# Optimization experiments

Measured on AMD Instinct MI355X. Metric: run time of the kernel, lower is better.

Reference implementation:

```python
import jax, jax.numpy as jnp
import numpy as np

D_MODEL = 1024
HEADS = 16
HEAD_DIM = D_MODEL // HEADS


def setup_inputs() -> dict:
    key = jax.random.key(0)
    k_x, k_q, k_k, k_v, k_o = jax.random.split(key, 5)
    B, S = 4, 2048
    return {
        "x": jax.random.normal(k_x, (B, S, D_MODEL), dtype=jnp.float32),
        "W_q": jax.random.normal(k_q, (D_MODEL, D_MODEL), dtype=jnp.float32),
        "W_k": jax.random.normal(k_k, (D_MODEL, D_MODEL), dtype=jnp.float32),
        "W_v": jax.random.normal(k_v, (D_MODEL, D_MODEL), dtype=jnp.float32),
        "fc_out": jax.random.normal(k_o, (D_MODEL, D_MODEL), dtype=jnp.float32),
    }


def reference(x, W_q, W_k, W_v, fc_out):
    B, S, D = x.shape
    H, Hd = HEADS, HEAD_DIM
    # QKV projections (no bias)
    Q = jnp.matmul(x, W_q)  # [B,S,D]
    K = jnp.matmul(x, W_k)
    V = jnp.matmul(x, W_v)
    # split heads -> [B,H,S,Hd]
    Qh = Q.reshape(B, S, H, Hd).transpose(0, 2, 1, 3)
    Kh = K.reshape(B, S, H, Hd).transpose(0, 2, 1, 3)
    Vh = V.reshape(B, S, H, Hd).transpose(0, 2, 1, 3)
    # full unfused attention: materialize [B,H,S,S] scores, softmax over last dim
    scores = jnp.einsum("bhqd,bhkd->bhqk", Qh, Kh) / jnp.sqrt(jnp.float32(Hd))
    attn = jax.nn.softmax(scores, axis=-1)
    head_out = jnp.einsum("bhqk,bhkd->bhqd", attn, Vh)  # [B,H,S,Hd]
    merged = head_out.transpose(0, 2, 1, 3).reshape(B, S, D)
    return jnp.matmul(merged, fc_out)
```

## Files before the change

kernel.cpp:

```cpp
#include <hip/hip_runtime.h>
#include <stdint.h>

#define MROWS 8192
#define DM    1024
#define NH    16
#define HD    64
#define SEQ   2048

typedef __bf16 bf16x8 __attribute__((ext_vector_type(8)));
typedef __bf16 bf16x4 __attribute__((ext_vector_type(4)));
typedef float  floatx4 __attribute__((ext_vector_type(4)));

#define QSCALE 0.18033688011112042f

__device__ __forceinline__ void async16(const void* g, void* l) {
  __builtin_amdgcn_global_load_lds(
      (__attribute__((address_space(1))) void*)g,
      (__attribute__((address_space(3))) void*)l,
      16, 0, 0);
}

__device__ __forceinline__ floatx4 mfma16(bf16x8 a, bf16x8 b, floatx4 c) {
  return __builtin_amdgcn_mfma_f32_16x16x32_bf16(a, b, c, 0, 0, 0);
}


__global__ void __launch_bounds__(256) split_x_kernel(const float* __restrict__ x,
                                                      __bf16* __restrict__ xh,
                                                      __bf16* __restrict__ xl) {
  const int i = blockIdx.x * 256 + threadIdx.x;
  const float4 v = reinterpret_cast<const float4*>(x)[i];
  const float vv[4] = {v.x, v.y, v.z, v.w};
  bf16x4 H, L;
#pragma unroll
  for (int j = 0; j < 4; ++j) {
    const __bf16 h = (__bf16)vv[j];
    H[j] = h;
    L[j] = (__bf16)(vv[j] - (float)h);
  }
  reinterpret_cast<bf16x4*>(xh)[i] = H;
  reinterpret_cast<bf16x4*>(xl)[i] = L;
}

__global__ void __launch_bounds__(256) wtrans_kernel(const float* __restrict__ W,
                                                     __bf16* __restrict__ Th,
                                                     __bf16* __restrict__ Tl) {
  __shared__ float t[32][33];
  const int tx = threadIdx.x & 31, ty = threadIdx.x >> 5;
  const int bx = blockIdx.x & 31, by = blockIdx.x >> 5;
#pragma unroll
  for (int j = 0; j < 4; ++j) {
    const int k = by * 32 + ty + j * 8;
    t[ty + j * 8][tx] = W[(size_t)k * DM + bx * 32 + tx];
  }
  __syncthreads();
#pragma unroll
  for (int j = 0; j < 4; ++j) {
    const int n = bx * 32 + ty + j * 8;
    const int k = by * 32 + tx;
    const float v = t[tx][ty + j * 8];
    const __bf16 h = (__bf16)v;
    Th[(size_t)n * DM + k] = h;
    if (Tl) Tl[(size_t)n * DM + k] = (__bf16)(v - (float)h);
  }
}

template <int OUTMODE>
__global__ void __launch_bounds__(256) gemm_nt(const __bf16* __restrict__ Ah,
                                               const __bf16* __restrict__ Bh,
                                               void* __restrict__ C0) {
  __shared__ __align__(16) __bf16 sAh[128 * 32];
  __shared__ __align__(16) __bf16 sBh[128 * 32];

  const int tid = threadIdx.x;
  const int bm = blockIdx.x >> 3;
  const int bn = blockIdx.x & 7;
  const int m0 = bm << 7, n0 = bn << 7;
  const int w = tid >> 6;
  const int lane = tid & 63;
  const int wm = (w >> 1) << 6;
  const int wn = (w & 1) << 6;
  const int lm = lane & 15;
  const int q4 = lane >> 4;

  floatx4 acc[4][4];
  const floatx4 fz = {0.f, 0.f, 0.f, 0.f};
#pragma unroll
  for (int i = 0; i < 4; ++i)
#pragma unroll
    for (int j = 0; j < 4; ++j) acc[i][j] = fz;

  const int c0 = tid, c1 = tid + 256;
  const int row0 = c0 >> 2, cc0 = (c0 & 3) ^ ((row0 >> 1) & 3);
  const int row1 = c1 >> 2, cc1 = (c1 & 3) ^ ((row1 >> 1) & 3);

  int offA[4], offB[4];
#pragma unroll
  for (int i = 0; i < 4; ++i) {
    const int ra = wm + i * 16 + lm;
    offA[i] = ra * 32 + ((q4 ^ ((ra >> 1) & 3)) << 3);
    const int rb = wn + i * 16 + lm;
    offB[i] = rb * 32 + ((q4 ^ ((rb >> 1) & 3)) << 3);
  }

  size_t ga0 = (size_t)(m0 + row0) * DM + cc0 * 8;
  size_t gb0 = (size_t)(n0 + row0) * DM + cc0 * 8;
  size_t ga1 = (size_t)(m0 + row1) * DM + cc1 * 8;
  size_t gb1 = (size_t)(n0 + row1) * DM + cc1 * 8;

  for (int it = 0; it < 32; ++it) {
    async16(Ah + ga0, &sAh[c0 * 8]);
    async16(Bh + gb0, &sBh[c0 * 8]);
    async16(Ah + ga1, &sAh[c1 * 8]);
    async16(Bh + gb1, &sBh[c1 * 8]);
    ga0 += 32; gb0 += 32; ga1 += 32; gb1 += 32;
    __syncthreads();

    bf16x8 ah[4], bh[4];
#pragma unroll
    for (int i = 0; i < 4; ++i) {
      ah[i] = *(const bf16x8*)&sAh[offA[i]];
      bh[i] = *(const bf16x8*)&sBh[offB[i]];
    }
#pragma unroll
    for (int i = 0; i < 4; ++i)
#pragma unroll
      for (int j = 0; j < 4; ++j)
        acc[i][j] = mfma16(ah[i], bh[j], acc[i][j]);
    __syncthreads();
  }

#pragma unroll
  for (int i = 0; i < 4; ++i) {
#pragma unroll
    for (int j = 0; j < 4; ++j) {
#pragma unroll
      for (int r = 0; r < 4; ++r) {
        const int gr = m0 + wm + i * 16 + q4 * 4 + r;
        const int gc = n0 + wn + j * 16 + lm;
        const float v = acc[i][j][r];
        if constexpr (OUTMODE == 1) {
          ((float*)C0)[(size_t)gr * DM + gc] = v;
        } else {
          const int bb = gr >> 11, ss = gr & 2047;
          const int s6 = ss & 63;
          const int sp = (ss & ~63) | (s6 & 32) | ((s6 & 12) << 1) |
                         ((s6 & 16) >> 2) | (s6 & 3);
          const int hh = gc >> 6, dd = gc & 63;
          ((__bf16*)C0)[(((size_t)(bb * NH + hh) << 6) + dd) * SEQ + sp] = (__bf16)v;
        }
      }
    }
  }
}

__global__ void __launch_bounds__(256, 2) gemm_qk(const __bf16* __restrict__ Ah,
                                                  const __bf16* __restrict__ Al,
                                                  const __bf16* __restrict__ Bqh,
                                                  const __bf16* __restrict__ Bql,
                                                  const __bf16* __restrict__ Bkh,
                                                  const __bf16* __restrict__ Bkl,
                                                  __bf16* __restrict__ Qh,
                                                  __bf16* __restrict__ Ql,
                                                  __bf16* __restrict__ Kh,
                                                  __bf16* __restrict__ Kl) {
  __shared__ __align__(16) __bf16 sAh[128 * 32];
  __shared__ __align__(16) __bf16 sAl[128 * 32];
  __shared__ __align__(16) __bf16 sQh_[128 * 32];
  __shared__ __align__(16) __bf16 sQl_[128 * 32];
  __shared__ __align__(16) __bf16 sKh_[128 * 32];
  __shared__ __align__(16) __bf16 sKl_[128 * 32];

  const int tid = threadIdx.x;
  const int bm = blockIdx.x >> 3;
  const int bn = blockIdx.x & 7;
  const int m0 = bm << 7, n0 = bn << 7;
  const int w = tid >> 6;
  const int lane = tid & 63;
  const int wm = (w >> 1) << 6;
  const int wn = (w & 1) << 6;
  const int lm = lane & 15;
  const int q4 = lane >> 4;

  floatx4 accq[4][4], acck[4][4];
  const floatx4 fz = {0.f, 0.f, 0.f, 0.f};
#pragma unroll
  for (int i = 0; i < 4; ++i)
#pragma unroll
    for (int j = 0; j < 4; ++j) { accq[i][j] = fz; acck[i][j] = fz; }

  const int c0 = tid, c1 = tid + 256;
  const int row0 = c0 >> 2, cc0 = (c0 & 3) ^ ((row0 >> 1) & 3);
  const int row1 = c1 >> 2, cc1 = (c1 & 3) ^ ((row1 >> 1) & 3);

  int offA[4], offB[4];
#pragma unroll
  for (int i = 0; i < 4; ++i) {
    const int ra = wm + i * 16 + lm;
    offA[i] = ra * 32 + ((q4 ^ ((ra >> 1) & 3)) << 3);
    const int rb = wn + i * 16 + lm;
    offB[i] = rb * 32 + ((q4 ^ ((rb >> 1) & 3)) << 3);
  }

  size_t ga0 = (size_t)(m0 + row0) * DM + cc0 * 8;
  size_t gb0 = (size_t)(n0 + row0) * DM + cc0 * 8;
  size_t ga1 = (size_t)(m0 + row1) * DM + cc1 * 8;
  size_t gb1 = (size_t)(n0 + row1) * DM + cc1 * 8;

  for (int it = 0; it < 32; ++it) {
    async16(Ah + ga0, &sAh[c0 * 8]);
    async16(Al + ga0, &sAl[c0 * 8]);
    async16(Ah + ga1, &sAh[c1 * 8]);
    async16(Al + ga1, &sAl[c1 * 8]);
    async16(Bqh + gb0, &sQh_[c0 * 8]);
    async16(Bql + gb0, &sQl_[c0 * 8]);
    async16(Bqh + gb1, &sQh_[c1 * 8]);
    async16(Bql + gb1, &sQl_[c1 * 8]);
    async16(Bkh + gb0, &sKh_[c0 * 8]);
    async16(Bkl + gb0, &sKl_[c0 * 8]);
    async16(Bkh + gb1, &sKh_[c1 * 8]);
    async16(Bkl + gb1, &sKl_[c1 * 8]);
    ga0 += 32; gb0 += 32; ga1 += 32; gb1 += 32;
    __syncthreads();

    bf16x8 ah[4], al[4];
#pragma unroll
    for (int i = 0; i < 4; ++i) {
      ah[i] = *(const bf16x8*)&sAh[offA[i]];
      al[i] = *(const bf16x8*)&sAl[offA[i]];
    }
    {
      bf16x8 bh[4], bl[4];
#pragma unroll
      for (int j = 0; j < 4; ++j) {
        bh[j] = *(const bf16x8*)&sQh_[offB[j]];
        bl[j] = *(const bf16x8*)&sQl_[offB[j]];
      }
#pragma unroll
      for (int i = 0; i < 4; ++i)
#pragma unroll
        for (int j = 0; j < 4; ++j) {
          accq[i][j] = mfma16(ah[i], bh[j], accq[i][j]);
          accq[i][j] = mfma16(ah[i], bl[j], accq[i][j]);
          accq[i][j] = mfma16(al[i], bh[j], accq[i][j]);
        }
    }
    {
      bf16x8 bh[4], bl[4];
#pragma unroll
      for (int j = 0; j < 4; ++j) {
        bh[j] = *(const bf16x8*)&sKh_[offB[j]];
        bl[j] = *(const bf16x8*)&sKl_[offB[j]];
      }
#pragma unroll
      for (int i = 0; i < 4; ++i)
#pragma unroll
        for (int j = 0; j < 4; ++j) {
          acck[i][j] = mfma16(ah[i], bh[j], acck[i][j]);
          acck[i][j] = mfma16(ah[i], bl[j], acck[i][j]);
          acck[i][j] = mfma16(al[i], bh[j], acck[i][j]);
        }
    }
    __syncthreads();
  }

#pragma unroll
  for (int i = 0; i < 4; ++i) {
#pragma unroll
    for (int j = 0; j < 4; ++j) {
#pragma unroll
      for (int r = 0; r < 4; ++r) {
        const int gr = m0 + wm + i * 16 + q4 * 4 + r;
        const int gc = n0 + wn + j * 16 + lm;
        const size_t idx = (size_t)gr * DM + gc;
        const float vq = accq[i][j][r] * QSCALE;
        const __bf16 qhv = (__bf16)vq;
        Qh[idx] = qhv;
        Ql[idx] = (__bf16)(vq - (float)qhv);
        const float vk = acck[i][j][r];
        const __bf16 khv = (__bf16)vk;
        Kh[idx] = khv;
        Kl[idx] = (__bf16)(vk - (float)khv);
      }
    }
  }
}

__global__ void __launch_bounds__(256, 3) flash_kernel(const __bf16* __restrict__ Qh,
                                                       const __bf16* __restrict__ Ql,
                                                       const __bf16* __restrict__ Kh,
                                                       const __bf16* __restrict__ Kl,
                                                       const __bf16* __restrict__ Vt,
                                                       __bf16* __restrict__ Mg) {
  __shared__ __align__(16) __bf16 sKh[2][64 * 64];
  __shared__ __align__(16) __bf16 sKl[2][64 * 64];
  __shared__ __align__(16) __bf16 sV[2][64 * 64];

  const int tid = threadIdx.x;
  const int qt = blockIdx.x & 15;
  const int bh = blockIdx.x >> 4;
  const int b = bh >> 4;
  const int h = bh & 15;
  const int mq0 = b * SEQ + qt * 128;
  const int ch = h * 64;
  const int w = tid >> 6;
  const int lane = tid & 63;
  const int lm = lane & 15;
  const int q4 = lane >> 4;

  const int c0 = tid, c1 = tid + 256;
  const int r0 = c0 >> 3, e0 = ((c0 & 7) ^ (r0 & 7)) << 3;
  const int r1 = c1 >> 3, e1 = ((c1 & 7) ^ (r1 & 7)) << 3;

  bf16x8 qh[2][2], ql[2][2];
#pragma unroll
  for (int p = 0; p < 2; ++p) {
    const size_t gq0 = (size_t)(mq0 + p * 64 + r0) * DM + ch + e0;
    const size_t gq1 = (size_t)(mq0 + p * 64 + r1) * DM + ch + e1;
    async16(Qh + gq0, &sKh[0][c0 * 8]);
    async16(Ql + gq0, &sKl[0][c0 * 8]);
    async16(Qh + gq1, &sKh[0][c1 * 8]);
    async16(Ql + gq1, &sKl[0][c1 * 8]);
    __syncthreads();
    if ((w >> 1) == p) {
#pragma unroll
      for (int mi = 0; mi < 2; ++mi) {
        const int rq = (w & 1) * 32 + mi * 16 + lm;
#pragma unroll
        for (int ks = 0; ks < 2; ++ks) {
          const int oq = rq * 64 + (((ks * 4 + q4) ^ (rq & 7)) << 3);
          qh[mi][ks] = *(const bf16x8*)&sKh[0][oq];
          ql[mi][ks] = *(const bf16x8*)&sKl[0][oq];
        }
      }
    }
    __syncthreads();
  }

  int ofr[2][4];
#pragma unroll
  for (int ks = 0; ks < 2; ++ks)
#pragma unroll
    for (int t = 0; t < 4; ++t) {
      const int rk = t * 16 + lm;
      ofr[ks][t] = rk * 64 + (((ks * 4 + q4) ^ (rk & 7)) << 3);
    }

  floatx4 o[2][4];
  const floatx4 fz = {0.f, 0.f, 0.f, 0.f};
#pragma unroll
  for (int mi = 0; mi < 2; ++mi)
#pragma unroll
    for (int dt = 0; dt < 4; ++dt) o[mi][dt] = fz;
  float lsum[2] = {0.f, 0.f};
  float m[2] = {-1e30f, -1e30f};

  size_t gk0 = (size_t)(b * SEQ + r0) * DM + ch + e0;
  size_t gk1 = (size_t)(b * SEQ + r1) * DM + ch + e1;
  size_t gv0 = (size_t)(bh * 64 + r0) * SEQ + e0;
  size_t gv1 = (size_t)(bh * 64 + r1) * SEQ + e1;

  async16(Kh + gk0, &sKh[0][c0 * 8]);
  async16(Kl + gk0, &sKl[0][c0 * 8]);
  async16(Kh + gk1, &sKh[0][c1 * 8]);
  async16(Kl + gk1, &sKl[0][c1 * 8]);
  async16(Vt + gv0, &sV[0][c0 * 8]);
  async16(Vt + gv1, &sV[0][c1 * 8]);
  gk0 += (size_t)64 * DM;
  gk1 += (size_t)64 * DM;
  gv0 += 64;
  gv1 += 64;

  for (int it = 0; it < 32; ++it) {
    const int cur = it & 1;
    asm volatile("s_waitcnt vmcnt(0)" ::: "memory");
    __builtin_amdgcn_s_barrier();
    __builtin_amdgcn_sched_barrier(0);
    if (it < 31) {
      const int nxt = cur ^ 1;
      async16(Kh + gk0, &sKh[nxt][c0 * 8]);
      async16(Kl + gk0, &sKl[nxt][c0 * 8]);
      async16(Kh + gk1, &sKh[nxt][c1 * 8]);
      async16(Kl + gk1, &sKl[nxt][c1 * 8]);
      async16(Vt + gv0, &sV[nxt][c0 * 8]);
      async16(Vt + gv1, &sV[nxt][c1 * 8]);
      gk0 += (size_t)64 * DM;
      gk1 += (size_t)64 * DM;
      gv0 += 64;
      gv1 += 64;
    }
    const __bf16* bKh = sKh[cur];
    const __bf16* bKl = sKl[cur];
    const __bf16* bV = sV[cur];

    floatx4 s2[4][2];
#pragma unroll
    for (int nt = 0; nt < 4; ++nt)
#pragma unroll
      for (int mi = 0; mi < 2; ++mi) s2[nt][mi] = fz;
#pragma unroll
    for (int ks = 0; ks < 2; ++ks) {
#pragma unroll
      for (int nt = 0; nt < 4; ++nt) {
        const bf16x8 kh = *(const bf16x8*)&bKh[ofr[ks][nt]];
        const bf16x8 kl = *(const bf16x8*)&bKl[ofr[ks][nt]];
#pragma unroll
        for (int mi = 0; mi < 2; ++mi) {
          s2[nt][mi] = mfma16(kh, qh[mi][ks], s2[nt][mi]);
          s2[nt][mi] = mfma16(kl, qh[mi][ks], s2[nt][mi]);
          s2[nt][mi] = mfma16(kh, ql[mi][ks], s2[nt][mi]);
        }
      }
    }

    float tm[2];
#pragma unroll
    for (int mi = 0; mi < 2; ++mi) {
      float mx = fmaxf(fmaxf(s2[0][mi][0], s2[0][mi][1]),
                       fmaxf(s2[0][mi][2], s2[0][mi][3]));
#pragma unroll
      for (int nt = 1; nt < 4; ++nt) {
        mx = fmaxf(mx, fmaxf(fmaxf(s2[nt][mi][0], s2[nt][mi][1]),
                             fmaxf(s2[nt][mi][2], s2[nt][mi][3])));
      }
      mx = fmaxf(mx, __shfl_xor(mx, 16));
      mx = fmaxf(mx, __shfl_xor(mx, 32));
      tm[mi] = mx;
    }
    if (__ballot((tm[0] > m[0] + 8.f) || (tm[1] > m[1] + 8.f))) {
#pragma unroll
      for (int mi = 0; mi < 2; ++mi) {
        const float mn = fmaxf(m[mi], tm[mi]);
        const float a = __builtin_amdgcn_exp2f(m[mi] - mn);
        m[mi] = mn;
        lsum[mi] *= a;
#pragma unroll
        for (int dt = 0; dt < 4; ++dt) o[mi][dt] *= a;
      }
    }

    bf16x8 aP[2][2];
#pragma unroll
    for (int mi = 0; mi < 2; ++mi) {
      float ps = 0.f;
#pragma unroll
      for (int nt = 0; nt < 4; ++nt) {
#pragma unroll
        for (int r = 0; r < 4; ++r) {
          const float p = __builtin_amdgcn_exp2f(s2[nt][mi][r] - m[mi]);
          ps += p;
          aP[mi][nt >> 1][(nt & 1) * 4 + r] = (__bf16)p;
        }
      }
      ps += __shfl_xor(ps, 16);
      ps += __shfl_xor(ps, 32);
      lsum[mi] += ps;
    }

#pragma unroll
    for (int ks = 0; ks < 2; ++ks) {
#pragma unroll
      for (int dt = 0; dt < 4; ++dt) {
        const bf16x8 bv = *(const bf16x8*)&bV[ofr[ks][dt]];
        o[0][dt] = mfma16(bv, aP[0][ks], o[0][dt]);
        o[1][dt] = mfma16(bv, aP[1][ks], o[1][dt]);
      }
    }
  }

#pragma unroll
  for (int mi = 0; mi < 2; ++mi) {
    const float inv = __builtin_amdgcn_rcpf(lsum[mi]);
    const int gr = mq0 + w * 32 + mi * 16 + lm;
#pragma unroll
    for (int dt = 0; dt < 4; ++dt) {
      bf16x4 ov;
#pragma unroll
      for (int r = 0; r < 4; ++r) ov[r] = (__bf16)(o[mi][dt][r] * inv);
      *(bf16x4*)&Mg[(size_t)gr * DM + ch + dt * 16 + q4 * 4] = ov;
    }
  }
}


extern "C" void kernel_launch(void* const* d_in, const int* in_sizes, int n_in,
                              void* d_out, int out_size, void* d_ws, size_t ws_size,
                              hipStream_t stream) {
  (void)in_sizes; (void)n_in; (void)out_size; (void)ws_size;
  const float* x  = (const float*)d_in[0];
  const float* Wq = (const float*)d_in[1];
  const float* Wk = (const float*)d_in[2];
  const float* Wv = (const float*)d_in[3];
  const float* fc = (const float*)d_in[4];
  float* out = (float*)d_out;

  char* base = (char*)d_ws;
  const size_t XB = (size_t)MROWS * DM * 2;
  const size_t WB = (size_t)DM * DM * 2;
  __bf16* xh  = (__bf16*)(base);
  __bf16* xl  = (__bf16*)(base + XB);
  __bf16* wqh = (__bf16*)(base + 2 * XB);
  __bf16* wql = (__bf16*)(base + 2 * XB + WB);
  __bf16* wkh = (__bf16*)(base + 2 * XB + 2 * WB);
  __bf16* wkl = (__bf16*)(base + 2 * XB + 3 * WB);
  __bf16* wvh = (__bf16*)(base + 2 * XB + 4 * WB);
  __bf16* fch = (__bf16*)(base + 2 * XB + 5 * WB);
  __bf16* Qh  = (__bf16*)(base + 2 * XB + 6 * WB);
  __bf16* Ql  = (__bf16*)(base + 3 * XB + 6 * WB);
  __bf16* Kh  = (__bf16*)(base + 4 * XB + 6 * WB);
  __bf16* Kl  = (__bf16*)(base + 5 * XB + 6 * WB);
  __bf16* Vt  = xl;
  __bf16* Mg  = xh;

  split_x_kernel<<<dim3(8192), dim3(256), 0, stream>>>(x, xh, xl);
  wtrans_kernel<<<dim3(1024), dim3(256), 0, stream>>>(Wq, wqh, wql);
  wtrans_kernel<<<dim3(1024), dim3(256), 0, stream>>>(Wk, wkh, wkl);
  wtrans_kernel<<<dim3(1024), dim3(256), 0, stream>>>(Wv, wvh, (__bf16*)nullptr);
  wtrans_kernel<<<dim3(1024), dim3(256), 0, stream>>>(fc, fch, (__bf16*)nullptr);

  gemm_qk<<<dim3(512), dim3(256), 0, stream>>>(xh, xl, wqh, wql, wkh, wkl, Qh, Ql, Kh, Kl);
  gemm_nt<3><<<dim3(512), dim3(256), 0, stream>>>(xh, wvh, (void*)Vt);

  flash_kernel<<<dim3(1024), dim3(256), 0, stream>>>(Qh, Ql, Kh, Kl, Vt, Mg);

  gemm_nt<1><<<dim3(512), dim3(256), 0, stream>>>(Mg, fch, (void*)out);
}
```

Before: 419.9 us.

## Double flash-attention query tile per block to share K/V tiles across eight waves

The flash kernel now runs 512 threads (8 waves) per block, with each block covering 256 query rows instead of 128, and the grid is halved to 512 blocks. Each staged K/V tile in LDS is consumed by twice as many waves, which halves global K/V traffic per query and simplifies loading to one 16-byte async copy per thread per buffer. The launch bound changes to (512, 6). That is a much higher occupancy request and may cap VGPRs enough to cause spills in the register-heavy split-precision inner loop. Fewer blocks also means coarser work distribution across CUs.

```diff
diff --git a/kernel.cpp b/kernel.cpp
--- a/kernel.cpp
+++ b/kernel.cpp
@@ -286,7 +286,7 @@
   }
 }
 
-__global__ void __launch_bounds__(256, 3) flash_kernel(const __bf16* __restrict__ Qh,
+__global__ void __launch_bounds__(512, 6) flash_kernel(const __bf16* __restrict__ Qh,
                                                        const __bf16* __restrict__ Ql,
                                                        const __bf16* __restrict__ Kh,
                                                        const __bf16* __restrict__ Kl,
@@ -297,30 +297,25 @@
   __shared__ __align__(16) __bf16 sV[2][64 * 64];
 
   const int tid = threadIdx.x;
-  const int qt = blockIdx.x & 15;
-  const int bh = blockIdx.x >> 4;
+  const int qt = blockIdx.x & 7;
+  const int bh = blockIdx.x >> 3;
   const int b = bh >> 4;
   const int h = bh & 15;
-  const int mq0 = b * SEQ + qt * 128;
+  const int mq0 = b * SEQ + qt * 256;
   const int ch = h * 64;
   const int w = tid >> 6;
   const int lane = tid & 63;
   const int lm = lane & 15;
   const int q4 = lane >> 4;
 
-  const int c0 = tid, c1 = tid + 256;
-  const int r0 = c0 >> 3, e0 = ((c0 & 7) ^ (r0 & 7)) << 3;
-  const int r1 = c1 >> 3, e1 = ((c1 & 7) ^ (r1 & 7)) << 3;
+  const int r0 = tid >> 3, e0 = ((tid & 7) ^ (r0 & 7)) << 3;
 
   bf16x8 qh[2][2], ql[2][2];
 #pragma unroll
-  for (int p = 0; p < 2; ++p) {
-    const size_t gq0 = (size_t)(mq0 + p * 64 + r0) * DM + ch + e0;
-    const size_t gq1 = (size_t)(mq0 + p * 64 + r1) * DM + ch + e1;
-    async16(Qh + gq0, &sKh[0][c0 * 8]);
-    async16(Ql + gq0, &sKl[0][c0 * 8]);
-    async16(Qh + gq1, &sKh[0][c1 * 8]);
-    async16(Ql + gq1, &sKl[0][c1 * 8]);
+  for (int p = 0; p < 4; ++p) {
+    const size_t gq = (size_t)(mq0 + p * 64 + r0) * DM + ch + e0;
+    async16(Qh + gq, &sKh[0][tid * 8]);
+    async16(Ql + gq, &sKl[0][tid * 8]);
     __syncthreads();
     if ((w >> 1) == p) {
 #pragma unroll
@@ -355,21 +350,14 @@
   float lsum[2] = {0.f, 0.f};
   float m[2] = {-1e30f, -1e30f};
 
-  size_t gk0 = (size_t)(b * SEQ + r0) * DM + ch + e0;
-  size_t gk1 = (size_t)(b * SEQ + r1) * DM + ch + e1;
-  size_t gv0 = (size_t)(bh * 64 + r0) * SEQ + e0;
-  size_t gv1 = (size_t)(bh * 64 + r1) * SEQ + e1;
-
-  async16(Kh + gk0, &sKh[0][c0 * 8]);
-  async16(Kl + gk0, &sKl[0][c0 * 8]);
-  async16(Kh + gk1, &sKh[0][c1 * 8]);
-  async16(Kl + gk1, &sKl[0][c1 * 8]);
-  async16(Vt + gv0, &sV[0][c0 * 8]);
-  async16(Vt + gv1, &sV[0][c1 * 8]);
-  gk0 += (size_t)64 * DM;
-  gk1 += (size_t)64 * DM;
-  gv0 += 64;
-  gv1 += 64;
+  size_t gk = (size_t)(b * SEQ + r0) * DM + ch + e0;
+  size_t gv = (size_t)(bh * 64 + r0) * SEQ + e0;
+
+  async16(Kh + gk, &sKh[0][tid * 8]);
+  async16(Kl + gk, &sKl[0][tid * 8]);
+  async16(Vt + gv, &sV[0][tid * 8]);
+  gk += (size_t)64 * DM;
+  gv += 64;
 
   for (int it = 0; it < 32; ++it) {
     const int cur = it & 1;
@@ -378,16 +366,11 @@
     __builtin_amdgcn_sched_barrier(0);
     if (it < 31) {
       const int nxt = cur ^ 1;
-      async16(Kh + gk0, &sKh[nxt][c0 * 8]);
-      async16(Kl + gk0, &sKl[nxt][c0 * 8]);
-      async16(Kh + gk1, &sKh[nxt][c1 * 8]);
-      async16(Kl + gk1, &sKl[nxt][c1 * 8]);
-      async16(Vt + gv0, &sV[nxt][c0 * 8]);
-      async16(Vt + gv1, &sV[nxt][c1 * 8]);
-      gk0 += (size_t)64 * DM;
-      gk1 += (size_t)64 * DM;
-      gv0 += 64;
-      gv1 += 64;
+      async16(Kh + gk, &sKh[nxt][tid * 8]);
+      async16(Kl + gk, &sKl[nxt][tid * 8]);
+      async16(Vt + gv, &sV[nxt][tid * 8]);
+      gk += (size_t)64 * DM;
+      gv += 64;
     }
     const __bf16* bKh = sKh[cur];
     const __bf16* bKl = sKl[cur];
@@ -521,7 +504,7 @@
   gemm_qk<<<dim3(512), dim3(256), 0, stream>>>(xh, xl, wqh, wql, wkh, wkl, Qh, Ql, Kh, Kl);
   gemm_nt<3><<<dim3(512), dim3(256), 0, stream>>>(xh, wvh, (void*)Vt);
 
-  flash_kernel<<<dim3(1024), dim3(256), 0, stream>>>(Qh, Ql, Kh, Kl, Vt, Mg);
+  flash_kernel<<<dim3(512), dim3(512), 0, stream>>>(Qh, Ql, Kh, Kl, Vt, Mg);
 
   gemm_nt<1><<<dim3(512), dim3(256), 0, stream>>>(Mg, fch, (void*)out);
 }
```

Measured after the change: 931.2 us. +121.8%, slower.
